# Optimization experiments

Hardware: AMD Instinct MI355X
Metric: run time of the kernel (lower is better)

Reference implementation:

```python
import jax, jax.numpy as jnp
import numpy as np
from math import log2, floor

B, N, DIM = 2, 2048, 2048
HEADS, DIM_HEAD, FF_MULT = 16, 128, 4
RMS_EPS = 1e-8


def _get_slopes(heads):
    def pow2_slopes(n):
        start = 2 ** (-2 ** (-(log2(n) - 3)))
        return [start * start ** i for i in range(n)]
    if log2(heads).is_integer():
        return pow2_slopes(heads)
    closest = 2 ** floor(log2(heads))
    return pow2_slopes(closest) + pow2_slopes(2 * closest)[0::2][: heads - closest]


def setup_inputs() -> dict:
    key = jax.random.key(0)
    ks = jax.random.split(key, 5)
    std = 0.02
    return {
        "x": jax.random.normal(ks[0], (B, N, DIM), dtype=jnp.float32),
        "g": jnp.ones((DIM,), dtype=jnp.float32),
        "w_qkv": jax.random.normal(ks[1], (DIM, DIM + DIM_HEAD), dtype=jnp.float32) * std,
        "w_attn_out": jax.random.normal(ks[2], (DIM, DIM), dtype=jnp.float32) * std,
        "w_ff1": jax.random.normal(ks[3], (DIM, 2 * FF_MULT * DIM), dtype=jnp.float32) * std,
        "w_ff2": jax.random.normal(ks[4], (FF_MULT * DIM, DIM), dtype=jnp.float32) * std,
    }


def reference(x, g, w_qkv, w_attn_out, w_ff1, w_ff2):
    b, n, dim = x.shape
    # RMSNorm: x / clamp(||x|| * dim^-0.5, eps) * g
    norm = jnp.linalg.norm(x, axis=-1, keepdims=True) * (dim ** -0.5)
    xn = x / jnp.maximum(norm, RMS_EPS) * g

    # Parallel SwiGLU FFN branch (shares normed input with attention)
    h = xn @ w_ff1                       # [b, n, 2*ff_mult*dim]
    val, gate = jnp.split(h, 2, axis=-1)
    ff_out = (jax.nn.silu(gate) * val) @ w_ff2  # [b, n, dim]

    # Multi-query attention: single dim_head-wide kv shared as K and V
    qkv = xn @ w_qkv                     # [b, n, dim + dim_head]
    q, kv = qkv[..., :dim], qkv[..., dim:]
    q = q.reshape(b, n, HEADS, DIM_HEAD) * (DIM_HEAD ** -0.5)
    sim = jnp.einsum('bihd,bjd->bhij', q, kv)  # [b, h, n, n]

    # ALiBi bias: -|j - i| * slope_h
    slopes = jnp.asarray(_get_slopes(HEADS), dtype=sim.dtype)[:, None, None]
    pos = jnp.arange(n)
    bias = -jnp.abs(pos[None, None, :] - pos[None, :, None]).astype(sim.dtype) * slopes
    sim = sim + bias

    # Causal mask (strict upper triangle masked)
    causal = jnp.triu(jnp.ones((n, n), dtype=bool), 1)
    neg = jnp.asarray(jnp.finfo(sim.dtype).max, sim.dtype)
    sim = jnp.where(causal, -neg, sim)

    attn = jax.nn.softmax(sim, axis=-1)
    out = jnp.einsum('bhij,bjd->bhid', attn, kv)     # [b, h, n, dim_head]
    out = out.transpose(0, 2, 1, 3).reshape(b, n, dim)
    return out @ w_attn_out + ff_out
```

## Files before the change

### kernel.cpp

```cpp
#include <hip/hip_runtime.h>
#include <stdint.h>

typedef unsigned short u16;
typedef __attribute__((ext_vector_type(8))) short bf16x8;
typedef __attribute__((ext_vector_type(4))) float f32x4;
typedef __attribute__((ext_vector_type(8))) unsigned short us8;
typedef __attribute__((ext_vector_type(4))) float fvec4;

#define BATCH 2
#define SEQ   2048
#define DIMM  2048
#define NH    16
#define DH    128
#define ROWS  (BATCH*SEQ)
#define QKVN  (DIMM + DH)
#define FFH   8192
#define LOG2E 1.44269504088896340736f

static __device__ __forceinline__ u16 f2bf(float x) {
  union { float f; uint32_t u; } v; v.f = x;
  uint32_t r = (v.u + 0x7fffu + ((v.u >> 16) & 1u)) >> 16;
  return (u16)r;
}

static __device__ __forceinline__ float fast_exp2(float x) {
  float r; asm("v_exp_f32 %0, %1" : "=v"(r) : "v"(x)); return r;
}

static __device__ __forceinline__ void gld_lds16(const void* g, void* l) {
  __builtin_amdgcn_global_load_lds(
      (const __attribute__((address_space(1))) uint32_t*)g,
      (__attribute__((address_space(3))) uint32_t*)l, 16, 0, 0);
}

__global__ __launch_bounds__(256)
void rmsnorm_k(const float* __restrict__ x, const float* __restrict__ g, u16* __restrict__ xn) {
  const int row = blockIdx.x;
  const float* xr = x + (size_t)row * DIMM;
  const int off = threadIdx.x * 8;
  fvec4 a = *(const fvec4*)(xr + off);
  fvec4 b = *(const fvec4*)(xr + off + 4);
  float ss = a[0]*a[0]+a[1]*a[1]+a[2]*a[2]+a[3]*a[3]
           + b[0]*b[0]+b[1]*b[1]+b[2]*b[2]+b[3]*b[3];
  #pragma unroll
  for (int m = 32; m >= 1; m >>= 1) ss += __shfl_xor(ss, m);
  __shared__ float red[4];
  if ((threadIdx.x & 63) == 0) red[threadIdx.x >> 6] = ss;
  __syncthreads();
  float tot = red[0] + red[1] + red[2] + red[3];
  float inv = 1.0f / fmaxf(sqrtf(tot * (1.0f / DIMM)), 1e-8f);
  fvec4 ga = *(const fvec4*)(g + off);
  fvec4 gb = *(const fvec4*)(g + off + 4);
  us8 o;
  #pragma unroll
  for (int i = 0; i < 4; i++) { o[i] = f2bf(a[i]*inv*ga[i]); o[4+i] = f2bf(b[i]*inv*gb[i]); }
  *(us8*)(xn + (size_t)row * DIMM + off) = o;
}

template<typename TIN>
__global__ __launch_bounds__(256)
void transpose_to_bf16(const TIN* __restrict__ in, u16* __restrict__ out, int R, int C) {
  __shared__ u16 tile[64 * 65];
  const int r0 = blockIdx.y * 64, c0 = blockIdx.x * 64;
  const int tr = threadIdx.x >> 2;
  const int tc = (threadIdx.x & 3) * 16;
  const TIN* ip = in + (size_t)(r0 + tr) * C + c0 + tc;
  u16 tmp[16];
  #pragma unroll
  for (int i = 0; i < 16; i++) {
    if constexpr (sizeof(TIN) == 4) tmp[i] = f2bf(((const float*)ip)[i]);
    else                            tmp[i] = ((const u16*)ip)[i];
  }
  #pragma unroll
  for (int i = 0; i < 16; i++) tile[tr * 65 + tc + i] = tmp[i];
  __syncthreads();
  const int oc  = c0 + tr;
  const int orr = (threadIdx.x & 3) * 16;
  us8 v0, v1;
  #pragma unroll
  for (int i = 0; i < 8; i++) v0[i] = tile[(orr + i) * 65 + tr];
  #pragma unroll
  for (int i = 0; i < 8; i++) v1[i] = tile[(orr + 8 + i) * 65 + tr];
  u16* op = out + (size_t)oc * R + r0 + orr;
  *(us8*)op = v0;
  *(us8*)(op + 8) = v1;
}

template<int MODE>
__global__ __launch_bounds__(256, 2)
void gemm_bf16(const u16* __restrict__ A, const u16* __restrict__ BT, int K,
               float* __restrict__ outF, u16* __restrict__ outQ, u16* __restrict__ outKV) {
  __shared__ __align__(16) u16 lA[128 * 32];
  __shared__ __align__(16) u16 lB[128 * 32];
  const int tid = threadIdx.x;
  const int wave = tid >> 6, lane = tid & 63;
  const int lid = lane & 15, quad = lane >> 4;
  const int wm = wave >> 1, wn = wave & 1;
  const int row0 = blockIdx.y * 128;
  const int col0 = blockIdx.x * 128;
  f32x4 acc[4][4];
  #pragma unroll
  for (int i = 0; i < 4; i++)
    #pragma unroll
    for (int j = 0; j < 4; j++) { acc[i][j][0]=0.f; acc[i][j][1]=0.f; acc[i][j][2]=0.f; acc[i][j][3]=0.f; }

  const int rA0 = wave * 32;
  const int rsub = lane >> 2;
  const int cl = lane & 3;

  for (int k0 = 0; k0 < K; k0 += 32) {
    #pragma unroll
    for (int h2 = 0; h2 < 2; ++h2) {
      int rloc = rA0 + h2 * 16 + rsub;
      int gc = cl ^ ((rloc >> 1) & 3);
      gld_lds16(A  + (size_t)(row0 + rloc) * K + k0 + gc * 8, lA + (rA0 + h2 * 16) * 32);
      gld_lds16(BT + (size_t)(col0 + rloc) * K + k0 + gc * 8, lB + (rA0 + h2 * 16) * 32);
    }
    __syncthreads();
    bf16x8 af[4], bfr[4];
    #pragma unroll
    for (int i = 0; i < 4; i++) {
      int r  = wm * 64 + i * 16 + lid;
      af[i]  = *(const bf16x8*)(lA + r * 32 + (quad ^ ((r >> 1) & 3)) * 8);
      int rb = wn * 64 + i * 16 + lid;
      bfr[i] = *(const bf16x8*)(lB + rb * 32 + (quad ^ ((rb >> 1) & 3)) * 8);
    }
    #pragma unroll
    for (int im = 0; im < 4; im++)
      #pragma unroll
      for (int in = 0; in < 4; in++)
        acc[im][in] = __builtin_amdgcn_mfma_f32_16x16x32_bf16(af[im], bfr[in], acc[im][in], 0, 0, 0);
    __syncthreads();
  }

  #pragma unroll
  for (int im = 0; im < 4; im++)
    #pragma unroll
    for (int in = 0; in < 4; in++) {
      int col = col0 + wn * 64 + in * 16 + lid;
      int rbase = row0 + wm * 64 + im * 16 + quad * 4;
      #pragma unroll
      for (int rg = 0; rg < 4; rg++) {
        float v = acc[im][in][rg];
        int row = rbase + rg;
        if constexpr (MODE == 0) {
          if (col < DIMM) outQ[(size_t)row * DIMM + col] = f2bf(v);
          else            outKV[(size_t)row * DH + (col - DIMM)] = f2bf(v);
        } else if constexpr (MODE == 2) {
          outF[(size_t)row * DIMM + col] = v;
        } else {
          outF[(size_t)row * DIMM + col] += v;
        }
      }
    }
}

__global__ __launch_bounds__(256, 2)
void gemm_ff1_swiglu(const u16* __restrict__ A, const u16* __restrict__ BT, u16* __restrict__ FF) {
  __shared__ __align__(16) u16 lA[128 * 32];
  __shared__ __align__(16) u16 lB[128 * 32];
  const int tid = threadIdx.x;
  const int wave = tid >> 6, lane = tid & 63;
  const int lid = lane & 15, quad = lane >> 4;
  const int wm = wave >> 1, wn = wave & 1;
  const int row0 = blockIdx.y * 128;
  const int n0 = blockIdx.x * 64;
  const int K = DIMM;
  f32x4 av[4][2], ag[4][2];
  #pragma unroll
  for (int i = 0; i < 4; i++)
    #pragma unroll
    for (int j = 0; j < 2; j++) {
      av[i][j][0]=0.f; av[i][j][1]=0.f; av[i][j][2]=0.f; av[i][j][3]=0.f;
      ag[i][j][0]=0.f; ag[i][j][1]=0.f; ag[i][j][2]=0.f; ag[i][j][3]=0.f;
    }
  const int rA0 = wave * 32;
  const int rsub = lane >> 2, cl = lane & 3;

  for (int k0 = 0; k0 < K; k0 += 32) {
    #pragma unroll
    for (int h2 = 0; h2 < 2; ++h2) {
      int rloc = rA0 + h2 * 16 + rsub;
      int gc = cl ^ ((rloc >> 1) & 3);
      int grow = (rloc < 64) ? (n0 + rloc) : (FFH + n0 + rloc - 64);
      gld_lds16(A  + (size_t)(row0 + rloc) * K + k0 + gc * 8, lA + (rA0 + h2 * 16) * 32);
      gld_lds16(BT + (size_t)grow * K + k0 + gc * 8,          lB + (rA0 + h2 * 16) * 32);
    }
    __syncthreads();
    bf16x8 af[4], bv[2], bg[2];
    #pragma unroll
    for (int i = 0; i < 4; i++) {
      int r = wm * 64 + i * 16 + lid;
      af[i] = *(const bf16x8*)(lA + r * 32 + (quad ^ ((r >> 1) & 3)) * 8);
    }
    #pragma unroll
    for (int i = 0; i < 2; i++) {
      int rv = wn * 32 + i * 16 + lid;
      bv[i] = *(const bf16x8*)(lB + rv * 32 + (quad ^ ((rv >> 1) & 3)) * 8);
      int rg2 = 64 + wn * 32 + i * 16 + lid;
      bg[i] = *(const bf16x8*)(lB + rg2 * 32 + (quad ^ ((rg2 >> 1) & 3)) * 8);
    }
    #pragma unroll
    for (int im = 0; im < 4; im++)
      #pragma unroll
      for (int in = 0; in < 2; in++) {
        av[im][in] = __builtin_amdgcn_mfma_f32_16x16x32_bf16(af[im], bv[in], av[im][in], 0, 0, 0);
        ag[im][in] = __builtin_amdgcn_mfma_f32_16x16x32_bf16(af[im], bg[in], ag[im][in], 0, 0, 0);
      }
    __syncthreads();
  }

  #pragma unroll
  for (int im = 0; im < 4; im++)
    #pragma unroll
    for (int in = 0; in < 2; in++) {
      int col = n0 + wn * 32 + in * 16 + lid;
      int rbase = row0 + wm * 64 + im * 16 + quad * 4;
      #pragma unroll
      for (int rg = 0; rg < 4; rg++) {
        float vv = av[im][in][rg];
        float gg = ag[im][in][rg];
        float sig = 1.0f / (1.0f + fast_exp2(-gg * LOG2E));
        FF[(size_t)(rbase + rg) * FFH + col] = f2bf(vv * gg * sig);
      }
    }
}

__global__ __launch_bounds__(256, 1)
void attn_k2(const u16* __restrict__ qws, const u16* __restrict__ kvws,
             const u16* __restrict__ kvt, u16* __restrict__ attnws) {
  __shared__ __align__(16) u16 kvls[128 * 128];
  __shared__ __align__(16) u16 kvtls[128 * 128];
  __shared__ __align__(16) u16 plds[4][32][136];
  const int tid = threadIdx.x;
  const int wave = tid >> 6, lane = tid & 63;
  const int lid = lane & 15, quad = lane >> 4;
  const int hb = blockIdx.y;
  const int h = hb & (NH - 1), b = hb >> 4;
  const int pair = blockIdx.x;
  const float slope2 = fast_exp2(-0.5f * (float)(h + 1)) * LOG2E;
  const float scale2 = 0.08838834764831845f * LOG2E;
  const float NEG = -__builtin_inff();

  const u16* kvb  = kvws + (size_t)b * SEQ * DH;
  const u16* kvtb = kvt  + (size_t)b * DH * SEQ;

  #pragma unroll 1
  for (int tt = 0; tt < 2; tt++) {
    const int T = tt ? (15 - pair) : pair;
    const int rw = T * 128 + wave * 32;

    bf16x8 qf[2][4];
    #pragma unroll
    for (int ig = 0; ig < 2; ig++)
      #pragma unroll
      for (int ks = 0; ks < 4; ks++)
        qf[ig][ks] = *(const bf16x8*)(qws + (size_t)(b * SEQ + rw + ig * 16 + lid) * DIMM
                                       + h * DH + ks * 32 + quad * 8);
    float srow2[2][4];
    #pragma unroll
    for (int ig = 0; ig < 2; ig++)
      #pragma unroll
      for (int rg = 0; rg < 4; rg++)
        srow2[ig][rg] = slope2 * (float)(rw + ig * 16 + quad * 4 + rg);

    f32x4 o[2][8];
    #pragma unroll
    for (int ig = 0; ig < 2; ig++)
      #pragma unroll
      for (int nd = 0; nd < 8; nd++) { o[ig][nd][0]=0.f; o[ig][nd][1]=0.f; o[ig][nd][2]=0.f; o[ig][nd][3]=0.f; }
    float m2[2][4], l[2][4];
    #pragma unroll
    for (int ig = 0; ig < 2; ig++)
      #pragma unroll
      for (int rg = 0; rg < 4; rg++) { m2[ig][rg] = NEG; l[ig][rg] = 0.f; }

    const int njt = T + 1;
    #pragma unroll 1
    for (int jt = 0; jt < njt; jt++) {
      const int j0 = jt * 128;
      __syncthreads();
      {
        const int c = lane & 15;
        const int r4 = lane >> 4;
        #pragma unroll
        for (int it = 0; it < 8; it++) {
          const int r = wave * 32 + it * 4 + r4;
          const int gc = c ^ (r & 15);
          gld_lds16(kvb  + (size_t)(j0 + r) * DH + gc * 8,        kvls  + (wave * 32 + it * 4) * 128);
          gld_lds16(kvtb + (size_t)r * SEQ + j0 + gc * 8,         kvtls + (wave * 32 + it * 4) * 128);
        }
      }
      __syncthreads();

      const int rhi = rw + 31;
      const int nbmax = min(8, ((rhi - j0) >> 4) + 1);
      const int ks2max = (nbmax + 1) >> 1;

      float pvv[2][8][4];
      float mt[2][4];
      #pragma unroll
      for (int ig = 0; ig < 2; ig++)
        #pragma unroll
        for (int rg = 0; rg < 4; rg++) mt[ig][rg] = NEG;

      #pragma unroll
      for (int nb = 0; nb < 8; nb++) {
        if (nb < nbmax) {
          bf16x8 bk[4];
          #pragma unroll
          for (int ks = 0; ks < 4; ks++)
            bk[ks] = *(const bf16x8*)(kvls + (nb * 16 + lid) * 128 + (((ks * 4 + quad) ^ lid) << 3));
          f32x4 s0, s1;
          s0[0]=0.f;s0[1]=0.f;s0[2]=0.f;s0[3]=0.f;
          s1[0]=0.f;s1[1]=0.f;s1[2]=0.f;s1[3]=0.f;
          #pragma unroll
          for (int ks = 0; ks < 4; ks++) {
            s0 = __builtin_amdgcn_mfma_f32_16x16x32_bf16(qf[0][ks], bk[ks], s0, 0, 0, 0);
            s1 = __builtin_amdgcn_mfma_f32_16x16x32_bf16(qf[1][ks], bk[ks], s1, 0, 0, 0);
          }
          const int jl = j0 + nb * 16 + lid;
          const float sj = slope2 * (float)jl;
          #pragma unroll
          for (int rg = 0; rg < 4; rg++) {
            const int row0r = rw + quad * 4 + rg;
            float e0 = fmaf(s0[rg], scale2, sj) - srow2[0][rg];
            e0 = (jl <= row0r) ? e0 : NEG;
            pvv[0][nb][rg] = e0;
            mt[0][rg] = fmaxf(mt[0][rg], e0);
            float e1 = fmaf(s1[rg], scale2, sj) - srow2[1][rg];
            e1 = (jl <= row0r + 16) ? e1 : NEG;
            pvv[1][nb][rg] = e1;
            mt[1][rg] = fmaxf(mt[1][rg], e1);
          }
        }
      }

      float alpha[2][4];
      #pragma unroll
      for (int ig = 0; ig < 2; ig++)
        #pragma unroll
        for (int rg = 0; rg < 4; rg++) {
          float m = mt[ig][rg];
          m = fmaxf(m, __shfl_xor(m, 1));
          m = fmaxf(m, __shfl_xor(m, 2));
          m = fmaxf(m, __shfl_xor(m, 4));
          m = fmaxf(m, __shfl_xor(m, 8));
          float mn = fmaxf(m2[ig][rg], m);
          alpha[ig][rg] = fast_exp2(m2[ig][rg] - mn);
          m2[ig][rg] = mn;
        }

      float rs[2][4];
      #pragma unroll
      for (int ig = 0; ig < 2; ig++)
        #pragma unroll
        for (int rg = 0; rg < 4; rg++) rs[ig][rg] = 0.f;
      #pragma unroll
      for (int nb = 0; nb < 8; nb++) {
        if (nb < nbmax) {
          #pragma unroll
          for (int ig = 0; ig < 2; ig++)
            #pragma unroll
            for (int rg = 0; rg < 4; rg++) {
              float p = fast_exp2(pvv[ig][nb][rg] - m2[ig][rg]);
              rs[ig][rg] += p;
              plds[wave][ig * 16 + quad * 4 + rg][nb * 16 + lid] = f2bf(p);
            }
        }
      }
      if (nbmax & 1) {
        #pragma unroll
        for (int ig = 0; ig < 2; ig++)
          #pragma unroll
          for (int rg = 0; rg < 4; rg++)
            plds[wave][ig * 16 + quad * 4 + rg][nbmax * 16 + lid] = 0;
      }

      #pragma unroll
      for (int ig = 0; ig < 2; ig++)
        #pragma unroll
        for (int rg = 0; rg < 4; rg++) {
          float r = rs[ig][rg];
          r += __shfl_xor(r, 1);
          r += __shfl_xor(r, 2);
          r += __shfl_xor(r, 4);
          r += __shfl_xor(r, 8);
          l[ig][rg] = l[ig][rg] * alpha[ig][rg] + r;
        }
      #pragma unroll
      for (int ig = 0; ig < 2; ig++)
        #pragma unroll
        for (int nd = 0; nd < 8; nd++)
          #pragma unroll
          for (int rg = 0; rg < 4; rg++) o[ig][nd][rg] *= alpha[ig][rg];

      asm volatile("s_waitcnt lgkmcnt(0)" ::: "memory");
      #pragma unroll
      for (int ks2 = 0; ks2 < 4; ks2++) {
        if (ks2 < ks2max) {
          bf16x8 pa0 = *(const bf16x8*)&plds[wave][lid][ks2 * 32 + quad * 8];
          bf16x8 pa1 = *(const bf16x8*)&plds[wave][16 + lid][ks2 * 32 + quad * 8];
          #pragma unroll
          for (int nd = 0; nd < 8; nd++) {
            bf16x8 bv = *(const bf16x8*)(kvtls + (nd * 16 + lid) * 128 + (((ks2 * 4 + quad) ^ lid) << 3));
            o[0][nd] = __builtin_amdgcn_mfma_f32_16x16x32_bf16(pa0, bv, o[0][nd], 0, 0, 0);
            o[1][nd] = __builtin_amdgcn_mfma_f32_16x16x32_bf16(pa1, bv, o[1][nd], 0, 0, 0);
          }
        }
      }
    }

    #pragma unroll
    for (int ig = 0; ig < 2; ig++) {
      float inv[4];
      #pragma unroll
      for (int rg = 0; rg < 4; rg++) inv[rg] = 1.0f / l[ig][rg];
      #pragma unroll
      for (int nd = 0; nd < 8; nd++)
        #pragma unroll
        for (int rg = 0; rg < 4; rg++) {
          int row = rw + ig * 16 + quad * 4 + rg;
          attnws[(size_t)(b * SEQ + row) * DIMM + h * DH + nd * 16 + lid] =
              f2bf(o[ig][nd][rg] * inv[rg]);
        }
    }
  }
}

extern "C" void kernel_launch(void* const* d_in, const int* in_sizes, int n_in,
                              void* d_out, int out_size, void* d_ws, size_t ws_size,
                              hipStream_t stream) {
  (void)in_sizes; (void)n_in; (void)out_size; (void)ws_size;
  const float* x     = (const float*)d_in[0];
  const float* g     = (const float*)d_in[1];
  const float* w_qkv = (const float*)d_in[2];
  const float* w_ao  = (const float*)d_in[3];
  const float* w_ff1 = (const float*)d_in[4];
  const float* w_ff2 = (const float*)d_in[5];
  float* out = (float*)d_out;

  u16* ws = (u16*)d_ws;
  u16* xn     = ws;
  u16* wTqkv  = xn     + 8388608;
  u16* wTattn = wTqkv  + 4456448;
  u16* wTff1  = wTattn + 4194304;
  u16* wTff2  = wTff1  + 33554432;
  u16* ffin   = wTff2  + 16777216;
  u16* qws    = ffin   + 33554432;
  u16* kvws   = qws    + 8388608;
  u16* kvtws  = kvws   + 524288;
  u16* attnws = kvtws  + 524288;

  transpose_to_bf16<float><<<dim3(QKVN/64, DIMM/64), 256, 0, stream>>>(w_qkv, wTqkv, DIMM, QKVN);
  transpose_to_bf16<float><<<dim3(DIMM/64, DIMM/64), 256, 0, stream>>>(w_ao, wTattn, DIMM, DIMM);
  transpose_to_bf16<float><<<dim3((2*FFH)/64, DIMM/64), 256, 0, stream>>>(w_ff1, wTff1, DIMM, 2*FFH);
  transpose_to_bf16<float><<<dim3(DIMM/64, FFH/64), 256, 0, stream>>>(w_ff2, wTff2, FFH, DIMM);

  rmsnorm_k<<<ROWS, 256, 0, stream>>>(x, g, xn);

  gemm_bf16<0><<<dim3(QKVN/128, ROWS/128), 256, 0, stream>>>(xn, wTqkv, DIMM, nullptr, qws, kvws);

  transpose_to_bf16<u16><<<dim3(DH/64, SEQ/64), 256, 0, stream>>>(kvws, kvtws, SEQ, DH);
  transpose_to_bf16<u16><<<dim3(DH/64, SEQ/64), 256, 0, stream>>>(kvws + (size_t)SEQ*DH, kvtws + (size_t)DH*SEQ, SEQ, DH);

  attn_k2<<<dim3(8, NH*BATCH), 256, 0, stream>>>(qws, kvws, kvtws, attnws);

  gemm_ff1_swiglu<<<dim3(FFH/64, ROWS/128), 256, 0, stream>>>(xn, wTff1, ffin);
  gemm_bf16<2><<<dim3(DIMM/128, ROWS/128), 256, 0, stream>>>(ffin, wTff2, FFH, out, nullptr, nullptr);

  gemm_bf16<3><<<dim3(DIMM/128, ROWS/128), 256, 0, stream>>>(attnws, wTattn, DIMM, out, nullptr, nullptr);
}
```

Before: 1.035 ms.

## Rewrite FF1 SwiGLU GEMM as 8-wave 256x256 double-buffered pipelined kernel

Replaces the 128x128-tile FF1+SwiGLU GEMM with a 512-thread kernel computing 256 rows by 128 value and 128 gate columns per block. It uses a K-step of 64, double-buffered LDS staging interleaved with MFMA quadrants under barriers, XOR-swizzled LDS layout, s_setprio around MFMA bursts, and a block-index swizzle for L2 locality. The aim is higher arithmetic intensity and hiding global-to-LDS latency behind compute in the largest GEMM. In exchange it needs 128 KB of LDS and a large accumulator register footprint, which may limit occupancy, and the hand-tuned waitcnt/barrier schedule is fragile.

```diff
diff --git a/kernel.cpp b/kernel.cpp
--- a/kernel.cpp
+++ b/kernel.cpp
@@ -155,75 +155,153 @@
     }
 }
 
-__global__ __launch_bounds__(256, 2)
-void gemm_ff1_swiglu(const u16* __restrict__ A, const u16* __restrict__ BT, u16* __restrict__ FF) {
-  __shared__ __align__(16) u16 lA[128 * 32];
-  __shared__ __align__(16) u16 lB[128 * 32];
+static __device__ __forceinline__ void stage_half(const u16* __restrict__ src, u16* dst,
+                                                  int K, int sr, int sgc, int wave) {
+  gld_lds16(src + (size_t)sr * K + sgc,       dst + wave * 1024);
+  gld_lds16(src + (size_t)(sr + 8) * K + sgc, dst + wave * 1024 + 512);
+}
+
+static __device__ __forceinline__ void lda4(bf16x8 (&dst)[4][2], const u16* sAb,
+                                            int mh, int wm, int lid, int c0) {
+  #pragma unroll
+  for (int i = 0; i < 4; ++i) {
+    const u16* p = sAb + (mh * 128 + wm * 64 + i * 16 + lid) * 64;
+    dst[i][0] = *(const bf16x8*)(p + c0);
+    dst[i][1] = *(const bf16x8*)(p + (c0 ^ 32));
+  }
+}
+
+static __device__ __forceinline__ void ldb2(bf16x8 (&dst)[2][2], const u16* sBb,
+                                            int nh, int wn, int lid, int c0) {
+  #pragma unroll
+  for (int n = 0; n < 2; ++n) {
+    const u16* p = sBb + (nh * 128 + wn * 32 + n * 16 + lid) * 64;
+    dst[n][0] = *(const bf16x8*)(p + c0);
+    dst[n][1] = *(const bf16x8*)(p + (c0 ^ 32));
+  }
+}
+
+static __device__ __forceinline__ void quad16(f32x4 (&acc)[8][4], const bf16x8 (&af)[4][2],
+                                              const bf16x8 (&bf)[2][2], int mh, int nh) {
+  __builtin_amdgcn_s_setprio(1);
+  #pragma unroll
+  for (int i = 0; i < 4; ++i)
+    #pragma unroll
+    for (int n = 0; n < 2; ++n) {
+      f32x4 c = acc[mh * 4 + i][nh * 2 + n];
+      c = __builtin_amdgcn_mfma_f32_16x16x32_bf16(af[i][0], bf[n][0], c, 0, 0, 0);
+      c = __builtin_amdgcn_mfma_f32_16x16x32_bf16(af[i][1], bf[n][1], c, 0, 0, 0);
+      acc[mh * 4 + i][nh * 2 + n] = c;
+    }
+  __builtin_amdgcn_s_setprio(0);
+}
+
+__global__ __launch_bounds__(512, 2)
+void gemm_ff1_swiglu_8p(const u16* __restrict__ A, const u16* __restrict__ BT,
+                        u16* __restrict__ FF) {
+  __shared__ __align__(16) u16 sA[2][256 * 64];
+  __shared__ __align__(16) u16 sB[2][256 * 64];
   const int tid = threadIdx.x;
   const int wave = tid >> 6, lane = tid & 63;
   const int lid = lane & 15, quad = lane >> 4;
-  const int wm = wave >> 1, wn = wave & 1;
-  const int row0 = blockIdx.y * 128;
-  const int n0 = blockIdx.x * 64;
+  const int wm = wave >> 2, wn = wave & 3;
   const int K = DIMM;
-  f32x4 av[4][2], ag[4][2];
-  #pragma unroll
-  for (int i = 0; i < 4; i++)
-    #pragma unroll
-    for (int j = 0; j < 2; j++) {
-      av[i][j][0]=0.f; av[i][j][1]=0.f; av[i][j][2]=0.f; av[i][j][3]=0.f;
-      ag[i][j][0]=0.f; ag[i][j][1]=0.f; ag[i][j][2]=0.f; ag[i][j][3]=0.f;
-    }
-  const int rA0 = wave * 32;
-  const int rsub = lane >> 2, cl = lane & 3;
-
-  for (int k0 = 0; k0 < K; k0 += 32) {
-    #pragma unroll
-    for (int h2 = 0; h2 < 2; ++h2) {
-      int rloc = rA0 + h2 * 16 + rsub;
-      int gc = cl ^ ((rloc >> 1) & 3);
-      int grow = (rloc < 64) ? (n0 + rloc) : (FFH + n0 + rloc - 64);
-      gld_lds16(A  + (size_t)(row0 + rloc) * K + k0 + gc * 8, lA + (rA0 + h2 * 16) * 32);
-      gld_lds16(BT + (size_t)grow * K + k0 + gc * 8,          lB + (rA0 + h2 * 16) * 32);
-    }
-    __syncthreads();
-    bf16x8 af[4], bv[2], bg[2];
-    #pragma unroll
-    for (int i = 0; i < 4; i++) {
-      int r = wm * 64 + i * 16 + lid;
-      af[i] = *(const bf16x8*)(lA + r * 32 + (quad ^ ((r >> 1) & 3)) * 8);
-    }
-    #pragma unroll
-    for (int i = 0; i < 2; i++) {
-      int rv = wn * 32 + i * 16 + lid;
-      bv[i] = *(const bf16x8*)(lB + rv * 32 + (quad ^ ((rv >> 1) & 3)) * 8);
-      int rg2 = 64 + wn * 32 + i * 16 + lid;
-      bg[i] = *(const bf16x8*)(lB + rg2 * 32 + (quad ^ ((rg2 >> 1) & 3)) * 8);
-    }
-    #pragma unroll
-    for (int im = 0; im < 4; im++)
-      #pragma unroll
-      for (int in = 0; in < 2; in++) {
-        av[im][in] = __builtin_amdgcn_mfma_f32_16x16x32_bf16(af[im], bv[in], av[im][in], 0, 0, 0);
-        ag[im][in] = __builtin_amdgcn_mfma_f32_16x16x32_bf16(af[im], bg[in], ag[im][in], 0, 0, 0);
-      }
-    __syncthreads();
-  }
-
-  #pragma unroll
-  for (int im = 0; im < 4; im++)
-    #pragma unroll
-    for (int in = 0; in < 2; in++) {
-      int col = n0 + wn * 32 + in * 16 + lid;
-      int rbase = row0 + wm * 64 + im * 16 + quad * 4;
-      #pragma unroll
-      for (int rg = 0; rg < 4; rg++) {
-        float vv = av[im][in][rg];
-        float gg = ag[im][in][rg];
+
+  int orig = blockIdx.y * 64 + blockIdx.x;
+  int swz = (orig & 7) * 128 + (orig >> 3);
+  const int row0 = (swz >> 6) * 256;
+  const int n0 = (swz & 63) * 128;
+
+  const int sr  = wave * 16 + (lane >> 3);
+  const int sgc = (((lane & 7) ^ (lane >> 3)) << 3);
+  const int c0  = ((quad ^ (lid & 7)) << 3);
+
+  f32x4 acc[8][4];
+  #pragma unroll
+  for (int i = 0; i < 8; ++i)
+    #pragma unroll
+    for (int j = 0; j < 4; ++j) { acc[i][j][0]=0.f; acc[i][j][1]=0.f; acc[i][j][2]=0.f; acc[i][j][3]=0.f; }
+
+  #define STAGE_A(b, h, kt) stage_half(A  + (size_t)(row0 + (h)*128) * K + (kt)*64, &sA[b][(h)*8192], K, sr, sgc, wave)
+  #define STAGE_B(b, h, kt) stage_half(BT + (size_t)((h) ? (FFH + n0) : n0) * K + (kt)*64, &sB[b][(h)*8192], K, sr, sgc, wave)
+  #define BAR() __builtin_amdgcn_s_barrier()
+
+  STAGE_A(0, 0, 0); STAGE_A(0, 1, 0); STAGE_B(0, 0, 0); STAGE_B(0, 1, 0);
+  STAGE_A(1, 0, 1); STAGE_B(1, 0, 1); STAGE_B(1, 1, 1);
+  asm volatile("s_waitcnt vmcnt(6)" ::: "memory");
+  BAR();
+
+  const int niter = K / 128;
+  for (int I = 0; I < niter; ++I) {
+    const bool more = (I + 1 < niter);
+    const int kt1 = 2 * I + 1, kt2 = 2 * I + 2, kt3 = 2 * I + 3;
+    bf16x8 af[4][2], b0f[2][2], b1f[2][2];
+
+    lda4(af, sA[0], 0, wm, lid, c0);
+    ldb2(b0f, sB[0], 0, wn, lid, c0);
+    STAGE_A(1, 1, kt1);
+    BAR();
+    quad16(acc, af, b0f, 0, 0);
+    BAR();
+    ldb2(b1f, sB[0], 1, wn, lid, c0);
+    if (more) STAGE_A(0, 0, kt2);
+    BAR();
+    quad16(acc, af, b1f, 0, 1);
+    BAR();
+    lda4(af, sA[0], 1, wm, lid, c0);
+    if (more) STAGE_B(0, 0, kt2);
+    BAR();
+    quad16(acc, af, b1f, 1, 1);
+    BAR();
+    if (more) STAGE_B(0, 1, kt2);
+    BAR();
+    quad16(acc, af, b0f, 1, 0);
+    if (more) { asm volatile("s_waitcnt vmcnt(6)" ::: "memory"); }
+    else      { asm volatile("s_waitcnt vmcnt(0)" ::: "memory"); }
+    BAR();
+
+    lda4(af, sA[1], 0, wm, lid, c0);
+    ldb2(b0f, sB[1], 0, wn, lid, c0);
+    if (more) STAGE_A(0, 1, kt2);
+    BAR();
+    quad16(acc, af, b0f, 0, 0);
+    BAR();
+    ldb2(b1f, sB[1], 1, wn, lid, c0);
+    if (more) STAGE_A(1, 0, kt3);
+    BAR();
+    quad16(acc, af, b1f, 0, 1);
+    BAR();
+    lda4(af, sA[1], 1, wm, lid, c0);
+    if (more) STAGE_B(1, 0, kt3);
+    BAR();
+    quad16(acc, af, b1f, 1, 1);
+    BAR();
+    if (more) STAGE_B(1, 1, kt3);
+    BAR();
+    quad16(acc, af, b0f, 1, 0);
+    if (more) { asm volatile("s_waitcnt vmcnt(6)" ::: "memory"); }
+    BAR();
+  }
+
+  #undef STAGE_A
+  #undef STAGE_B
+  #undef BAR
+
+  #pragma unroll
+  for (int mi = 0; mi < 8; ++mi) {
+    const int row = row0 + (mi >> 2) * 128 + wm * 64 + (mi & 3) * 16 + quad * 4;
+    #pragma unroll
+    for (int n = 0; n < 2; ++n) {
+      const int col = n0 + wn * 32 + n * 16 + lid;
+      #pragma unroll
+      for (int rg = 0; rg < 4; ++rg) {
+        float vv = acc[mi][n][rg];
+        float gg = acc[mi][2 + n][rg];
         float sig = 1.0f / (1.0f + fast_exp2(-gg * LOG2E));
-        FF[(size_t)(rbase + rg) * FFH + col] = f2bf(vv * gg * sig);
-      }
-    }
+        FF[(size_t)(row + rg) * FFH + col] = f2bf(vv * gg * sig);
+      }
+    }
+  }
 }
 
 __global__ __launch_bounds__(256, 1)
@@ -466,7 +544,7 @@
 
   attn_k2<<<dim3(8, NH*BATCH), 256, 0, stream>>>(qws, kvws, kvtws, attnws);
 
-  gemm_ff1_swiglu<<<dim3(FFH/64, ROWS/128), 256, 0, stream>>>(xn, wTff1, ffin);
+  gemm_ff1_swiglu_8p<<<dim3(FFH/128, ROWS/256), 512, 0, stream>>>(xn, wTff1, ffin);
   gemm_bf16<2><<<dim3(DIMM/128, ROWS/128), 256, 0, stream>>>(ffin, wTff2, FFH, out, nullptr, nullptr);
 
   gemm_bf16<3><<<dim3(DIMM/128, ROWS/128), 256, 0, stream>>>(attnws, wTattn, DIMM, out, nullptr, nullptr);
```

New measurement: 1.004 ms. 3.0% less time.
